# Kernel tuning notes

Hardware: AMD Instinct MI355X
Metric: run time of the kernel (lower is better)

Reference implementation:

```python
import jax, jax.numpy as jnp
import numpy as np

N_NODES = 100000
N_EDGES = 1000000
N_REL = 200
D_IN = 64
D_OUT = 64


def setup_inputs() -> dict:
    key = jax.random.key(0)
    ks = jax.random.split(key, 12)
    scale = float(np.sqrt(6.0 / (D_IN + D_OUT)))  # xavier_uniform
    inp = {
        "node_feat": jax.random.normal(ks[0], (N_NODES, D_IN), dtype=jnp.float32),
        "rel_emb": jax.random.normal(ks[1], (N_REL, D_IN), dtype=jnp.float32),
        "src": jax.random.randint(ks[2], (N_EDGES,), 0, N_NODES, dtype=jnp.int32),
        "dst": jax.random.randint(ks[3], (N_EDGES,), 0, N_NODES, dtype=jnp.int32),
        "etype": jax.random.randint(ks[4], (N_EDGES,), 0, N_REL, dtype=jnp.int32),
        "direction": jax.random.randint(ks[5], (N_EDGES,), 0, 2, dtype=jnp.int32),
        "W_self": jax.random.uniform(ks[6], (D_OUT, D_IN), jnp.float32, -scale, scale),
        "W_forward": jax.random.uniform(ks[7], (D_OUT, D_IN), jnp.float32, -scale, scale),
        "W_backward": jax.random.uniform(ks[8], (D_OUT, D_IN), jnp.float32, -scale, scale),
        "W_rel": jax.random.uniform(ks[9], (D_OUT, D_IN), jnp.float32, -scale, scale),
        "bias": jnp.zeros((D_OUT,), dtype=jnp.float32),
    }
    return inp


def reference(node_feat, rel_emb, src, dst, etype, direction,
              W_self, W_forward, W_backward, W_rel, bias):
    # Gather: edge messages via 'sub' composition (h_src - r_etype). [E, D_in]
    msg = node_feat[src] - rel_emb[etype]
    # Direction-specific linear transform. Torch code only fills msg_transformed
    # for forward (direction==0) edges; backward edges contribute zeros.
    msg_t = msg @ W_forward.T  # [E, D_out]
    fwd_mask = (direction == 0)[:, None].astype(msg_t.dtype)
    msg_t = msg_t * fwd_mask
    # Scatter-reduce (sum) into destination nodes.
    h_neigh = jax.ops.segment_sum(msg_t, dst, num_segments=N_NODES)
    out = node_feat @ W_self.T + h_neigh + bias
    rel_out = rel_emb @ W_rel.T
    return out, rel_out
```

## Files before the change

### kernel.cpp

```cpp
#include <hip/hip_runtime.h>

#define D 64
#define SCAN_CHUNK 1024

typedef short bf16x8 __attribute__((ext_vector_type(8)));
typedef float f32x4 __attribute__((ext_vector_type(4)));

__device__ __forceinline__ short f2bf(float x) {
  unsigned u = __builtin_bit_cast(unsigned, x);
  u = u + 0x7FFFu + ((u >> 16) & 1u);
  return (short)(u >> 16);
}

__global__ __launch_bounds__(256) void rel_kernel(
    const float* __restrict__ rel_emb,
    const float* __restrict__ W_f,
    const float* __restrict__ W_rel,
    float* __restrict__ R,
    float* __restrict__ rel_out,
    int n_rel) {
  __shared__ float WtF[D][D];
  __shared__ float WtR[D][D];
  int tid = threadIdx.x;
  for (int idx = tid; idx < D * D; idx += 256) {
    int j = idx >> 6, k = idx & 63;
    WtF[k][j] = W_f[idx];
    WtR[k][j] = W_rel[idx];
  }
  __syncthreads();
  int lane = tid & 63, wave = tid >> 6;
  for (int r = blockIdx.x * 4 + wave; r < n_rel; r += gridDim.x * 4) {
    const float4* a = (const float4*)(rel_emb + (size_t)r * D);
    float accR = 0.f, accO = 0.f;
#pragma unroll
    for (int k4 = 0; k4 < 16; ++k4) {
      float4 av = a[k4];
      int k = k4 * 4;
      accR += av.x * WtF[k][lane] + av.y * WtF[k + 1][lane] +
              av.z * WtF[k + 2][lane] + av.w * WtF[k + 3][lane];
      accO += av.x * WtR[k][lane] + av.y * WtR[k + 1][lane] +
              av.z * WtR[k + 2][lane] + av.w * WtR[k + 3][lane];
    }
    R[(size_t)r * D + lane] = accR;
    rel_out[(size_t)r * D + lane] = accO;
  }
}

__global__ __launch_bounds__(256) void node_mfma(
    const float* __restrict__ nf,
    const float* __restrict__ W_self,
    const float* __restrict__ W_f,
    const float* __restrict__ bias,
    float* __restrict__ out,
    float* __restrict__ X,
    int n_nodes) {
  int tid = threadIdx.x;
  int lane = tid & 63;
  int l15 = lane & 15;
  int kg = lane >> 4;

  bf16x8 bS[4][2], bF[4][2];
#pragma unroll
  for (int q = 0; q < 4; ++q) {
#pragma unroll
    for (int h = 0; h < 2; ++h) {
      const float* ps = W_self + (size_t)(q * 16 + l15) * D + h * 32 + kg * 8;
      const float* pf = W_f + (size_t)(q * 16 + l15) * D + h * 32 + kg * 8;
      float4 s0 = *(const float4*)ps, s1 = *(const float4*)(ps + 4);
      float4 f0 = *(const float4*)pf, f1 = *(const float4*)(pf + 4);
      bf16x8 vs, vf;
      vs[0] = f2bf(s0.x); vs[1] = f2bf(s0.y); vs[2] = f2bf(s0.z); vs[3] = f2bf(s0.w);
      vs[4] = f2bf(s1.x); vs[5] = f2bf(s1.y); vs[6] = f2bf(s1.z); vs[7] = f2bf(s1.w);
      vf[0] = f2bf(f0.x); vf[1] = f2bf(f0.y); vf[2] = f2bf(f0.z); vf[3] = f2bf(f0.w);
      vf[4] = f2bf(f1.x); vf[5] = f2bf(f1.y); vf[6] = f2bf(f1.z); vf[7] = f2bf(f1.w);
      bS[q][h] = vs;
      bF[q][h] = vf;
    }
  }
  float bq[4];
#pragma unroll
  for (int q = 0; q < 4; ++q) bq[q] = bias[q * 16 + l15];

  int wave = (int)((blockIdx.x * blockDim.x + tid) >> 6);
  int n_waves = (int)((gridDim.x * blockDim.x) >> 6);
  int ntiles = (n_nodes + 15) >> 4;

  for (int t = wave; t < ntiles; t += n_waves) {
    int base = t << 4;
    int arow = base + l15;
    if (arow >= n_nodes) arow = n_nodes - 1;
    const float* ap = nf + (size_t)arow * D + kg * 8;
    float4 a00 = *(const float4*)ap;
    float4 a01 = *(const float4*)(ap + 4);
    float4 a10 = *(const float4*)(ap + 32);
    float4 a11 = *(const float4*)(ap + 36);
    bf16x8 af0, af1;
    af0[0] = f2bf(a00.x); af0[1] = f2bf(a00.y); af0[2] = f2bf(a00.z); af0[3] = f2bf(a00.w);
    af0[4] = f2bf(a01.x); af0[5] = f2bf(a01.y); af0[6] = f2bf(a01.z); af0[7] = f2bf(a01.w);
    af1[0] = f2bf(a10.x); af1[1] = f2bf(a10.y); af1[2] = f2bf(a10.z); af1[3] = f2bf(a10.w);
    af1[4] = f2bf(a11.x); af1[5] = f2bf(a11.y); af1[6] = f2bf(a11.z); af1[7] = f2bf(a11.w);

    bool full = (base + 16 <= n_nodes);
#pragma unroll
    for (int q = 0; q < 4; ++q) {
      f32x4 accS = {0.f, 0.f, 0.f, 0.f};
      f32x4 accF = {0.f, 0.f, 0.f, 0.f};
      accS = __builtin_amdgcn_mfma_f32_16x16x32_bf16(af0, bS[q][0], accS, 0, 0, 0);
      accS = __builtin_amdgcn_mfma_f32_16x16x32_bf16(af1, bS[q][1], accS, 0, 0, 0);
      accF = __builtin_amdgcn_mfma_f32_16x16x32_bf16(af0, bF[q][0], accF, 0, 0, 0);
      accF = __builtin_amdgcn_mfma_f32_16x16x32_bf16(af1, bF[q][1], accF, 0, 0, 0);
      int col = q * 16 + l15;
      int row0 = base + kg * 4;
      size_t o = (size_t)row0 * D + col;
      if (full) {
#pragma unroll
        for (int r = 0; r < 4; ++r) {
          out[o + (size_t)r * D] = accS[r] + bq[q];
          X[o + (size_t)r * D] = accF[r];
        }
      } else {
#pragma unroll
        for (int r = 0; r < 4; ++r) {
          if (row0 + r < n_nodes) {
            out[o + (size_t)r * D] = accS[r] + bq[q];
            X[o + (size_t)r * D] = accF[r];
          }
        }
      }
    }
  }
}

__global__ __launch_bounds__(256) void k_zero(int4* __restrict__ p, int n4) {
  int i = blockIdx.x * blockDim.x + threadIdx.x;
  int stride = gridDim.x * blockDim.x;
  int4 z = {0, 0, 0, 0};
  for (; i < n4; i += stride) p[i] = z;
}

__global__ __launch_bounds__(256) void k_hist(
    const int* __restrict__ dst, const int* __restrict__ dir,
    int* __restrict__ cnt, int n_edges) {
  int i = blockIdx.x * blockDim.x + threadIdx.x;
  int stride = gridDim.x * blockDim.x;
  for (; i < n_edges; i += stride)
    if (dir[i] == 0) atomicAdd(&cnt[dst[i]], 1);
}

__global__ __launch_bounds__(256) void k_sums(
    const int* __restrict__ cnt, int* __restrict__ sums, int n) {
  __shared__ int ws_[4];
  int b = blockIdx.x, t = threadIdx.x;
  int lane = t & 63, wave = t >> 6;
  int s = 0;
  for (int j = 0; j < 4; ++j) {
    int i = b * SCAN_CHUNK + t * 4 + j;
    if (i < n) s += cnt[i];
  }
  for (int off = 32; off; off >>= 1) s += __shfl_down(s, off);
  if (lane == 0) ws_[wave] = s;
  __syncthreads();
  if (t == 0) sums[b] = ws_[0] + ws_[1] + ws_[2] + ws_[3];
}

__global__ __launch_bounds__(256) void k_scan_chunks(
    int* __restrict__ cnt, const int* __restrict__ sums, int n) {
  __shared__ int wsum[4];
  __shared__ int off_s;
  int b = blockIdx.x, t = threadIdx.x;
  int lane = t & 63, wave = t >> 6;
  if (t < 64) {
    int v = 0;
    for (int i = t; i < b; i += 64) v += sums[i];
    for (int o = 32; o; o >>= 1) v += __shfl_down(v, o);
    if (t == 0) off_s = v;
  }
  int i0 = b * SCAN_CHUNK + t * 4;
  int c0 = (i0 + 0 < n) ? cnt[i0 + 0] : 0;
  int c1 = (i0 + 1 < n) ? cnt[i0 + 1] : 0;
  int c2 = (i0 + 2 < n) ? cnt[i0 + 2] : 0;
  int c3 = (i0 + 3 < n) ? cnt[i0 + 3] : 0;
  int s = c0 + c1 + c2 + c3;
  int inc = s;
  for (int d = 1; d < 64; d <<= 1) {
    int v = __shfl_up(inc, d);
    if (lane >= d) inc += v;
  }
  if (lane == 63) wsum[wave] = inc;
  __syncthreads();
  int wbase = 0;
  if (wave > 0) wbase += wsum[0];
  if (wave > 1) wbase += wsum[1];
  if (wave > 2) wbase += wsum[2];
  int ex = off_s + wbase + inc - s;
  if (i0 + 0 < n) cnt[i0 + 0] = ex;
  if (i0 + 1 < n) cnt[i0 + 1] = ex + c0;
  if (i0 + 2 < n) cnt[i0 + 2] = ex + c0 + c1;
  if (i0 + 3 < n) cnt[i0 + 3] = ex + c0 + c1 + c2;
}

__global__ __launch_bounds__(256) void k_scatter_packed(
    const int* __restrict__ src, const int* __restrict__ dst,
    const int* __restrict__ et, const int* __restrict__ dir,
    int* __restrict__ cursor, int* __restrict__ perm, int n_edges) {
  int i = blockIdx.x * blockDim.x + threadIdx.x;
  int stride = gridDim.x * blockDim.x;
  for (; i < n_edges; i += stride)
    if (dir[i] == 0) {
      int pos = atomicAdd(&cursor[dst[i]], 1);
      perm[pos] = (src[i] << 8) | et[i];
    }
}

__global__ __launch_bounds__(256) void k_gather(
    const int* __restrict__ cursor, const int* __restrict__ perm,
    const float* __restrict__ X, const float* __restrict__ R,
    float* __restrict__ out, int n_nodes) {
  int lane = threadIdx.x & 63;
  int wave_id = (int)((blockIdx.x * blockDim.x + threadIdx.x) >> 6);
  int n_waves = (int)((gridDim.x * blockDim.x) >> 6);
  for (int node = wave_id; node < n_nodes; node += n_waves) {
    int end = cursor[node];
    int beg = (node == 0) ? 0 : cursor[node - 1];
    if (end <= beg) continue;
    float acc = 0.f;
    int k = beg;
    for (; k + 3 < end; k += 4) {
      int p0 = perm[k], p1 = perm[k + 1], p2 = perm[k + 2], p3 = perm[k + 3];
      float a0 = X[(size_t)(p0 >> 8) * D + lane] - R[(size_t)(p0 & 255) * D + lane];
      float a1 = X[(size_t)(p1 >> 8) * D + lane] - R[(size_t)(p1 & 255) * D + lane];
      float a2 = X[(size_t)(p2 >> 8) * D + lane] - R[(size_t)(p2 & 255) * D + lane];
      float a3 = X[(size_t)(p3 >> 8) * D + lane] - R[(size_t)(p3 & 255) * D + lane];
      acc += (a0 + a1) + (a2 + a3);
    }
    for (; k < end; ++k) {
      int p = perm[k];
      acc += X[(size_t)(p >> 8) * D + lane] - R[(size_t)(p & 255) * D + lane];
    }
    out[(size_t)node * D + lane] += acc;
  }
}

__global__ __launch_bounds__(256) void edge_atomic(
    const int* __restrict__ src, const int* __restrict__ dst,
    const int* __restrict__ et, const int* __restrict__ dir,
    const float* __restrict__ X, const float* __restrict__ R,
    float* __restrict__ out, int n_edges) {
  int lane = threadIdx.x & 63;
  long long wave_id = ((long long)blockIdx.x * blockDim.x + threadIdx.x) >> 6;
  long long n_waves = ((long long)gridDim.x * blockDim.x) >> 6;
  for (long long base = wave_id * 64; base < n_edges; base += n_waves * 64) {
    int e = (int)base + lane;
    int s_l = 0, d_l = 0, t_l = 0, dir_l = 1;
    if (e < n_edges) {
      s_l = src[e]; d_l = dst[e]; t_l = et[e]; dir_l = dir[e];
    }
    int cnt = min(64, n_edges - (int)base);
    for (int i = 0; i < cnt; ++i) {
      int dir_i = __shfl(dir_l, i);
      if (dir_i != 0) continue;
      int s_i = __shfl(s_l, i);
      int t_i = __shfl(t_l, i);
      int d_i = __shfl(d_l, i);
      float val = X[(size_t)s_i * D + lane] - R[(size_t)t_i * D + lane];
      atomicAdd(&out[(size_t)d_i * D + lane], val);
    }
  }
}

extern "C" void kernel_launch(void* const* d_in, const int* in_sizes, int n_in,
                              void* d_out, int out_size, void* d_ws, size_t ws_size,
                              hipStream_t stream) {
  const float* node_feat = (const float*)d_in[0];
  const float* rel_emb   = (const float*)d_in[1];
  const int*   src       = (const int*)d_in[2];
  const int*   dst       = (const int*)d_in[3];
  const int*   etype     = (const int*)d_in[4];
  const int*   direction = (const int*)d_in[5];
  const float* W_self    = (const float*)d_in[6];
  const float* W_forward = (const float*)d_in[7];
  const float* W_rel     = (const float*)d_in[9];
  const float* bias      = (const float*)d_in[10];

  int n_nodes = in_sizes[0] / D;
  int n_rel   = in_sizes[1] / D;
  int n_edges = in_sizes[2];

  float* out     = (float*)d_out;
  float* rel_out = out + (size_t)n_nodes * D;

  char* ws = (char*)d_ws;
  size_t offX = 0;
  size_t offR = offX + (size_t)n_nodes * D * 4;
  size_t offCur = offR + (size_t)n_rel * D * 4;
  size_t offSums = offCur + (((size_t)n_nodes * 4 + 15) & ~(size_t)15);
  size_t offPerm = offSums + 1024 * 4;
  size_t need = offPerm + (size_t)n_edges * 4;

  float* X = (float*)(ws + offX);
  float* R = (float*)(ws + offR);
  int* cursor = (int*)(ws + offCur);
  int* sums = (int*)(ws + offSums);
  int* perm = (int*)(ws + offPerm);

  rel_kernel<<<50, 256, 0, stream>>>(rel_emb, W_forward, W_rel, R, rel_out, n_rel);

  int ntiles = (n_nodes + 15) / 16;
  int nblocks = (ntiles + 3) / 4;
  node_mfma<<<nblocks, 256, 0, stream>>>(node_feat, W_self, W_forward, bias,
                                         out, X, n_nodes);

  bool packed_ok = (n_rel <= 256) && (n_nodes < (1 << 23));
  if (ws_size >= need && packed_ok) {
    int nblk = (n_nodes + SCAN_CHUNK - 1) / SCAN_CHUNK;
    int n4 = (n_nodes + 3) / 4;
    k_zero<<<(n4 + 255) / 256, 256, 0, stream>>>((int4*)cursor, n4);
    k_hist<<<1024, 256, 0, stream>>>(dst, direction, cursor, n_edges);
    k_sums<<<nblk, 256, 0, stream>>>(cursor, sums, n_nodes);
    k_scan_chunks<<<nblk, 256, 0, stream>>>(cursor, sums, n_nodes);
    k_scatter_packed<<<1024, 256, 0, stream>>>(src, dst, etype, direction,
                                               cursor, perm, n_edges);
    k_gather<<<2048, 256, 0, stream>>>(cursor, perm, X, R, out, n_nodes);
  } else {
    edge_atomic<<<2048, 256, 0, stream>>>(src, dst, etype, direction, X, R, out,
                                          n_edges);
  }
}
```

Measured before the change: 139.9 us.

## Store gathered X and R intermediates in bf16, fuse cursor zeroing into rel kernel

The per-node transformed features X and relation projections R are now written as bf16 and widened back to fp32 inside the gather and atomic fallback kernels. This halves the bytes moved by the random-access edge gather and makes the X table more likely to stay cache-resident. The separate cursor-zeroing kernel is folded into rel_kernel, and node_mfma launches a fixed 512-block grid. In exchange, the messages lose precision through bf16 rounding of X and R before accumulation.

```diff
diff --git a/kernel.cpp b/kernel.cpp
--- a/kernel.cpp
+++ b/kernel.cpp
@@ -11,14 +11,25 @@
   u = u + 0x7FFFu + ((u >> 16) & 1u);
   return (short)(u >> 16);
 }
+__device__ __forceinline__ float bf2f(unsigned short u) {
+  unsigned v = ((unsigned)u) << 16;
+  return __builtin_bit_cast(float, v);
+}
 
 __global__ __launch_bounds__(256) void rel_kernel(
     const float* __restrict__ rel_emb,
     const float* __restrict__ W_f,
     const float* __restrict__ W_rel,
-    float* __restrict__ R,
+    unsigned short* __restrict__ R2,
     float* __restrict__ rel_out,
-    int n_rel) {
+    int n_rel,
+    int4* __restrict__ cz, int ncz4) {
+  {
+    int i = blockIdx.x * blockDim.x + threadIdx.x;
+    int stride = gridDim.x * blockDim.x;
+    int4 z = {0, 0, 0, 0};
+    for (; i < ncz4; i += stride) cz[i] = z;
+  }
   __shared__ float WtF[D][D];
   __shared__ float WtR[D][D];
   int tid = threadIdx.x;
@@ -41,7 +52,7 @@
       accO += av.x * WtR[k][lane] + av.y * WtR[k + 1][lane] +
               av.z * WtR[k + 2][lane] + av.w * WtR[k + 3][lane];
     }
-    R[(size_t)r * D + lane] = accR;
+    R2[(size_t)r * D + lane] = (unsigned short)f2bf(accR);
     rel_out[(size_t)r * D + lane] = accO;
   }
 }
@@ -52,7 +63,7 @@
     const float* __restrict__ W_f,
     const float* __restrict__ bias,
     float* __restrict__ out,
-    float* __restrict__ X,
+    unsigned short* __restrict__ X2,
     int n_nodes) {
   int tid = threadIdx.x;
   int lane = tid & 63;
@@ -116,26 +127,19 @@
 #pragma unroll
         for (int r = 0; r < 4; ++r) {
           out[o + (size_t)r * D] = accS[r] + bq[q];
-          X[o + (size_t)r * D] = accF[r];
+          X2[o + (size_t)r * D] = (unsigned short)f2bf(accF[r]);
         }
       } else {
 #pragma unroll
         for (int r = 0; r < 4; ++r) {
           if (row0 + r < n_nodes) {
             out[o + (size_t)r * D] = accS[r] + bq[q];
-            X[o + (size_t)r * D] = accF[r];
+            X2[o + (size_t)r * D] = (unsigned short)f2bf(accF[r]);
           }
         }
       }
     }
   }
-}
-
-__global__ __launch_bounds__(256) void k_zero(int4* __restrict__ p, int n4) {
-  int i = blockIdx.x * blockDim.x + threadIdx.x;
-  int stride = gridDim.x * blockDim.x;
-  int4 z = {0, 0, 0, 0};
-  for (; i < n4; i += stride) p[i] = z;
 }
 
 __global__ __launch_bounds__(256) void k_hist(
@@ -214,7 +218,7 @@
 
 __global__ __launch_bounds__(256) void k_gather(
     const int* __restrict__ cursor, const int* __restrict__ perm,
-    const float* __restrict__ X, const float* __restrict__ R,
+    const unsigned short* __restrict__ X2, const unsigned short* __restrict__ R2,
     float* __restrict__ out, int n_nodes) {
   int lane = threadIdx.x & 63;
   int wave_id = (int)((blockIdx.x * blockDim.x + threadIdx.x) >> 6);
@@ -227,15 +231,15 @@
     int k = beg;
     for (; k + 3 < end; k += 4) {
       int p0 = perm[k], p1 = perm[k + 1], p2 = perm[k + 2], p3 = perm[k + 3];
-      float a0 = X[(size_t)(p0 >> 8) * D + lane] - R[(size_t)(p0 & 255) * D + lane];
-      float a1 = X[(size_t)(p1 >> 8) * D + lane] - R[(size_t)(p1 & 255) * D + lane];
-      float a2 = X[(size_t)(p2 >> 8) * D + lane] - R[(size_t)(p2 & 255) * D + lane];
-      float a3 = X[(size_t)(p3 >> 8) * D + lane] - R[(size_t)(p3 & 255) * D + lane];
+      float a0 = bf2f(X2[(size_t)(p0 >> 8) * D + lane]) - bf2f(R2[(size_t)(p0 & 255) * D + lane]);
+      float a1 = bf2f(X2[(size_t)(p1 >> 8) * D + lane]) - bf2f(R2[(size_t)(p1 & 255) * D + lane]);
+      float a2 = bf2f(X2[(size_t)(p2 >> 8) * D + lane]) - bf2f(R2[(size_t)(p2 & 255) * D + lane]);
+      float a3 = bf2f(X2[(size_t)(p3 >> 8) * D + lane]) - bf2f(R2[(size_t)(p3 & 255) * D + lane]);
       acc += (a0 + a1) + (a2 + a3);
     }
     for (; k < end; ++k) {
       int p = perm[k];
-      acc += X[(size_t)(p >> 8) * D + lane] - R[(size_t)(p & 255) * D + lane];
+      acc += bf2f(X2[(size_t)(p >> 8) * D + lane]) - bf2f(R2[(size_t)(p & 255) * D + lane]);
     }
     out[(size_t)node * D + lane] += acc;
   }
@@ -244,7 +248,7 @@
 __global__ __launch_bounds__(256) void edge_atomic(
     const int* __restrict__ src, const int* __restrict__ dst,
     const int* __restrict__ et, const int* __restrict__ dir,
-    const float* __restrict__ X, const float* __restrict__ R,
+    const unsigned short* __restrict__ X2, const unsigned short* __restrict__ R2,
     float* __restrict__ out, int n_edges) {
   int lane = threadIdx.x & 63;
   long long wave_id = ((long long)blockIdx.x * blockDim.x + threadIdx.x) >> 6;
@@ -262,7 +266,7 @@
       int s_i = __shfl(s_l, i);
       int t_i = __shfl(t_l, i);
       int d_i = __shfl(d_l, i);
-      float val = X[(size_t)s_i * D + lane] - R[(size_t)t_i * D + lane];
+      float val = bf2f(X2[(size_t)s_i * D + lane]) - bf2f(R2[(size_t)t_i * D + lane]);
       atomicAdd(&out[(size_t)d_i * D + lane], val);
     }
   }
@@ -291,38 +295,39 @@
 
   char* ws = (char*)d_ws;
   size_t offX = 0;
-  size_t offR = offX + (size_t)n_nodes * D * 4;
-  size_t offCur = offR + (size_t)n_rel * D * 4;
+  size_t offR = offX + (size_t)n_nodes * D * 2;
+  size_t offCur = offR + (size_t)n_rel * D * 2;
+  offCur = (offCur + 15) & ~(size_t)15;
   size_t offSums = offCur + (((size_t)n_nodes * 4 + 15) & ~(size_t)15);
   size_t offPerm = offSums + 1024 * 4;
   size_t need = offPerm + (size_t)n_edges * 4;
 
-  float* X = (float*)(ws + offX);
-  float* R = (float*)(ws + offR);
+  unsigned short* X2 = (unsigned short*)(ws + offX);
+  unsigned short* R2 = (unsigned short*)(ws + offR);
   int* cursor = (int*)(ws + offCur);
   int* sums = (int*)(ws + offSums);
   int* perm = (int*)(ws + offPerm);
 
-  rel_kernel<<<50, 256, 0, stream>>>(rel_emb, W_forward, W_rel, R, rel_out, n_rel);
-
-  int ntiles = (n_nodes + 15) / 16;
-  int nblocks = (ntiles + 3) / 4;
-  node_mfma<<<nblocks, 256, 0, stream>>>(node_feat, W_self, W_forward, bias,
-                                         out, X, n_nodes);
-
   bool packed_ok = (n_rel <= 256) && (n_nodes < (1 << 23));
-  if (ws_size >= need && packed_ok) {
+  bool csr = (ws_size >= need) && packed_ok;
+  int ncz4 = csr ? (n_nodes + 3) / 4 : 0;
+
+  rel_kernel<<<64, 256, 0, stream>>>(rel_emb, W_forward, W_rel, R2, rel_out,
+                                     n_rel, (int4*)cursor, ncz4);
+
+  node_mfma<<<512, 256, 0, stream>>>(node_feat, W_self, W_forward, bias,
+                                     out, X2, n_nodes);
+
+  if (csr) {
     int nblk = (n_nodes + SCAN_CHUNK - 1) / SCAN_CHUNK;
-    int n4 = (n_nodes + 3) / 4;
-    k_zero<<<(n4 + 255) / 256, 256, 0, stream>>>((int4*)cursor, n4);
     k_hist<<<1024, 256, 0, stream>>>(dst, direction, cursor, n_edges);
     k_sums<<<nblk, 256, 0, stream>>>(cursor, sums, n_nodes);
     k_scan_chunks<<<nblk, 256, 0, stream>>>(cursor, sums, n_nodes);
     k_scatter_packed<<<1024, 256, 0, stream>>>(src, dst, etype, direction,
                                                cursor, perm, n_edges);
-    k_gather<<<2048, 256, 0, stream>>>(cursor, perm, X, R, out, n_nodes);
+    k_gather<<<2048, 256, 0, stream>>>(cursor, perm, X2, R2, out, n_nodes);
   } else {
-    edge_atomic<<<2048, 256, 0, stream>>>(src, dst, etype, direction, X, R, out,
-                                          n_edges);
-  }
-}
+    edge_atomic<<<2048, 256, 0, stream>>>(src, dst, etype, direction, X2, R2,
+                                          out, n_edges);
+  }
+}
```

Measured after the change: 124.5 us. 1.12x faster.
